# Kernel tuning notes

Hardware: AMD Instinct MI355X
Metric: run time of the kernel (lower is better)

Reference implementation:

```python
import jax, jax.numpy as jnp
import numpy as np

N_NODES = 100000
N_EDGES = 1000000
F_IN = 128
HID = 128
OUT = 64


def setup_inputs() -> dict:
    key = jax.random.key(0)
    ks = jax.random.split(key, 8)
    node_features = jax.random.normal(ks[0], (N_NODES, F_IN), dtype=jnp.float32)
    edge_index = jax.random.randint(ks[1], (2, N_EDGES), 0, N_NODES, dtype=jnp.int64)
    s1 = 1.0 / np.sqrt(F_IN)
    s2 = 1.0 / np.sqrt(HID)
    W1 = jax.random.uniform(ks[2], (F_IN, HID), jnp.float32, -s1, s1)
    b1 = jax.random.uniform(ks[3], (HID,), jnp.float32, -s1, s1)
    W2 = jax.random.uniform(ks[4], (HID, HID), jnp.float32, -s2, s2)
    b2 = jax.random.uniform(ks[5], (HID,), jnp.float32, -s2, s2)
    Wp = jax.random.uniform(ks[6], (HID, OUT), jnp.float32, -s2, s2)
    bp = jax.random.uniform(ks[7], (OUT,), jnp.float32, -s2, s2)
    return {"node_features": node_features, "edge_index": edge_index,
            "W1": W1, "b1": b1, "W2": W2, "b2": b2, "Wp": Wp, "bp": bp}


def reference(node_features, edge_index, W1, b1, W2, b2, Wp, bp):
    # encoder: Linear -> ReLU -> Linear
    h = jax.nn.relu(node_features @ W1 + b1) @ W2 + b2  # [N, HID]
    src = edge_index[0]
    dst = edge_index[1]
    # per-edge gather of h[src], scatter-add into dst (segment reduce)
    messages = jax.ops.segment_sum(h[src], dst, num_segments=h.shape[0])  # [N, HID]
    h = h + messages
    pooled = jnp.mean(h, axis=0)  # [HID]
    return pooled @ Wp + bp  # [OUT]
```

## Files before the change

### kernel.cpp

```cpp
#include <hip/hip_runtime.h>
#include <hip/hip_bf16.h>
#include <stdint.h>

typedef __attribute__((ext_vector_type(8))) short short8;
typedef __attribute__((ext_vector_type(4))) float f32x4;
typedef __attribute__((ext_vector_type(2))) float f32x2;
typedef __attribute__((ext_vector_type(4))) int i32x4;

#define NRANGE 4
#define RNODES 25600
#define RW     12800
#define NS     32
#define NFRAG  16

static __device__ __forceinline__ short to_bf16s(float f) {
  __hip_bfloat16 h = __float2bfloat16(f);
  return __builtin_bit_cast(short, h);
}

__global__ __launch_bounds__(1024) void k_histprep(
    const int* __restrict__ e, unsigned* __restrict__ priv,
    short* __restrict__ frag, const float* __restrict__ W1, int E) {
  __shared__ unsigned cnt[RW];
  __shared__ int is64s;
  int b = blockIdx.x, tid = threadIdx.x;
  if (b < NFRAG) {
    int idx = b * 1024 + tid;
    int k = idx >> 7, col = idx & 127;
    int ct = col >> 4, ks = k >> 5, lh = (k >> 3) & 3, ee = k & 7;
    int lane = lh * 16 + (col & 15);
    frag[((ct * 4 + ks) * 64 + lane) * 8 + ee] = to_bf16s(W1[idx]);
    return;
  }
  int h = b - NFRAG;
  int r = h / NS, s = h % NS;
  if (tid < 64) {
    unsigned long long bl = __ballot(e[2 * tid + 1] == 0);
    if (tid == 0) is64s = (__popcll(bl) > 32) ? 1 : 0;
  }
  for (int j = tid; j < RW; j += 1024) cnt[j] = 0u;
  __syncthreads();
  int is64 = is64s;
  unsigned base = (unsigned)r * RNODES;
  int nq = E >> 2;
  int qlo = (int)((long long)s * nq / NS);
  int qhi = (int)((long long)(s + 1) * nq / NS);
  for (int q = qlo + tid; q < qhi; q += 1024) {
    i32x4 v;
    if (is64) {
      i32x4 a = *reinterpret_cast<const i32x4*>(e + 8 * (size_t)q);
      i32x4 bb = *reinterpret_cast<const i32x4*>(e + 8 * (size_t)q + 4);
      v = i32x4{a[0], a[2], bb[0], bb[2]};
    } else {
      v = *reinterpret_cast<const i32x4*>(e + 4 * (size_t)q);
    }
#pragma unroll
    for (int k = 0; k < 4; ++k) {
      unsigned loc = (unsigned)v[k] - base;
      if (loc < (unsigned)RNODES)
        atomicAdd(&cnt[loc >> 1], 1u << (16 * (loc & 1)));
    }
  }
  if (s == 0) {
    int tail = E & 3;
    if (tid < tail) {
      int idx = E - tail + tid;
      unsigned loc = (unsigned)(is64 ? e[2 * idx] : e[idx]) - base;
      if (loc < (unsigned)RNODES)
        atomicAdd(&cnt[loc >> 1], 1u << (16 * (loc & 1)));
    }
  }
  __syncthreads();
  unsigned* dst = priv + (size_t)h * RW;
  for (int j = tid; j < RW; j += 1024) dst[j] = cnt[j];
}

__global__ __launch_bounds__(256) void k_merge(const unsigned* __restrict__ priv,
                                               float* __restrict__ wdeg, int N) {
  int g = blockIdx.x * 256 + threadIdx.x;
  if (g >= NRANGE * RW) return;
  int r = g / RW, word = g % RW;
  const unsigned* p = priv + (size_t)(r * NS) * RW + word;
  unsigned lo = 0, hi = 0;
#pragma unroll 8
  for (int s = 0; s < NS; ++s) {
    unsigned v = p[(size_t)s * RW];
    lo += v & 0xFFFFu;
    hi += v >> 16;
  }
  int n0 = r * RNODES + 2 * word;
  if (n0 + 1 < N) {
    *reinterpret_cast<f32x2*>(wdeg + n0) =
        f32x2{1.0f + (float)lo, 1.0f + (float)hi};
  } else if (n0 < N) {
    wdeg[n0] = 1.0f + (float)lo;
  }
}

__global__ __launch_bounds__(256) void k_main(
    const float* __restrict__ X, const short* __restrict__ w1frag,
    const float* __restrict__ b1, const float* __restrict__ wdeg,
    float* __restrict__ partials, int nNodes) {
  __shared__ __align__(16) short w1s[16384];
  __shared__ __align__(16) short xs[8192];
  __shared__ float wdeg_s[64];
  __shared__ float sred[128];

  int tid = threadIdx.x;
  {
    const f32x4* src = reinterpret_cast<const f32x4*>(w1frag);
    f32x4* dst = reinterpret_cast<f32x4*>(w1s);
#pragma unroll
    for (int i = 0; i < 8; ++i) dst[tid + i * 256] = src[tid + i * 256];
  }
  if (tid < 128) sred[tid] = 0.f;

  int lane = tid & 63, wave = tid >> 6;
  int rA = lane & 15;
  int kh = lane >> 4;

  float b1r[8];
#pragma unroll
  for (int ct = 0; ct < 8; ++ct) b1r[ct] = b1[ct * 16 + rA];

  float sl[8] = {0, 0, 0, 0, 0, 0, 0, 0};
  int nChunks = (nNodes + 63) >> 6;
  __syncthreads();

  for (int c = blockIdx.x; c < nChunks; c += gridDim.x) {
    int row0 = c << 6;
#pragma unroll
    for (int p = 0; p < 4; ++p) {
      int j = p * 256 + tid;
      int rl = j >> 4, kc = j & 15;
      int grow = row0 + rl;
      if (grow > nNodes - 1) grow = nNodes - 1;
      const f32x4* gp =
          reinterpret_cast<const f32x4*>(X + (size_t)grow * 128 + kc * 8);
      f32x4 lo = gp[0], hi = gp[1];
      short8 v;
#pragma unroll
      for (int ee = 0; ee < 4; ++ee) {
        v[ee] = to_bf16s(lo[ee]);
        v[4 + ee] = to_bf16s(hi[ee]);
      }
      int u = rl * 16 + (kc ^ (rl & 7));
      *reinterpret_cast<short8*>(&xs[u * 8]) = v;
    }
    if (tid < 64) {
      int row = row0 + tid;
      wdeg_s[tid] = (row < nNodes) ? wdeg[row] : 0.f;
    }
    __syncthreads();

    int rloc = wave * 16 + rA;
    f32x4 acc[8];
#pragma unroll
    for (int ct = 0; ct < 8; ++ct) acc[ct] = f32x4{0.f, 0.f, 0.f, 0.f};
#pragma unroll
    for (int ks = 0; ks < 4; ++ks) {
      int kc = ks * 4 + kh;
      int u = rloc * 16 + (kc ^ (rloc & 7));
      short8 a = *reinterpret_cast<const short8*>(&xs[u * 8]);
#pragma unroll
      for (int ct = 0; ct < 8; ++ct) {
        short8 bfr = *reinterpret_cast<const short8*>(
            &w1s[((ct * 4 + ks) * 64 + lane) * 8]);
        acc[ct] = __builtin_amdgcn_mfma_f32_16x16x32_bf16(a, bfr, acc[ct], 0, 0, 0);
      }
    }
#pragma unroll
    for (int rr = 0; rr < 4; ++rr) {
      int rl = wave * 16 + kh * 4 + rr;
      float w = wdeg_s[rl];
#pragma unroll
      for (int ct = 0; ct < 8; ++ct)
        sl[ct] += w * fmaxf(acc[ct][rr] + b1r[ct], 0.f);
    }
    __syncthreads();
  }

#pragma unroll
  for (int ct = 0; ct < 8; ++ct) {
    float v = sl[ct];
    v += __shfl_xor(v, 16);
    v += __shfl_xor(v, 32);
    if (kh == 0) atomicAdd(&sred[ct * 16 + rA], v);
  }
  __syncthreads();
  if (tid < 128) partials[(size_t)blockIdx.x * 128 + tid] = sred[tid];
}

__global__ __launch_bounds__(1024) void k_final(
    const float* __restrict__ partials, int B, const float* __restrict__ W2,
    const float* __restrict__ b2, const float* __restrict__ Wp,
    const float* __restrict__ bp, float* __restrict__ out,
    float totalW, float invN) {
  __shared__ float accsA[32 * 128];
  __shared__ float sv[128];
  __shared__ float pooled[128];
  int t = threadIdx.x;
  {
    int cg = t & 31, slc = t >> 5;
    f32x4 s = f32x4{0.f, 0.f, 0.f, 0.f};
#pragma unroll 4
    for (int r = slc; r < B; r += 32)
      s += *reinterpret_cast<const f32x4*>(partials + (size_t)r * 128 + cg * 4);
    *reinterpret_cast<f32x4*>(&accsA[slc * 128 + cg * 4]) = s;
  }
  __syncthreads();
  if (t < 128) {
    float v = 0.f;
#pragma unroll
    for (int i = 0; i < 32; ++i) v += accsA[i * 128 + t];
    sv[t] = v;
  }
  __syncthreads();
  {
    int col = t & 127, sl8 = t >> 7;
    float a = 0.f;
#pragma unroll
    for (int kk = 0; kk < 16; ++kk) {
      int k = sl8 * 16 + kk;
      a += sv[k] * W2[k * 128 + col];
    }
    accsA[sl8 * 128 + col] = a;
  }
  __syncthreads();
  if (t < 128) {
    float v = totalW * b2[t];
#pragma unroll
    for (int i = 0; i < 8; ++i) v += accsA[i * 128 + t];
    pooled[t] = v * invN;
  }
  __syncthreads();
  if (t < 512) {
    int o = t & 63, s2 = t >> 6;
    float a = 0.f;
#pragma unroll
    for (int kk = 0; kk < 16; ++kk) {
      int k = s2 * 16 + kk;
      a += pooled[k] * Wp[k * 64 + o];
    }
    accsA[s2 * 64 + o] = a;
  }
  __syncthreads();
  if (t < 64) {
    float v = bp[t];
#pragma unroll
    for (int i = 0; i < 8; ++i) v += accsA[i * 64 + t];
    out[t] = v;
  }
}

__global__ void k_zero(unsigned* __restrict__ p, int n) {
  int i = blockIdx.x * 256 + threadIdx.x;
  if (i < n) p[i] = 0u;
}
__global__ __launch_bounds__(256) void k_hist_fb(const int* __restrict__ e,
                                                 unsigned* __restrict__ deg,
                                                 int E) {
  __shared__ int is64s;
  int tid = threadIdx.x;
  if (tid < 64) {
    unsigned long long bl = __ballot(e[2 * tid + 1] == 0);
    if (tid == 0) is64s = (__popcll(bl) > 32) ? 1 : 0;
  }
  __syncthreads();
  int is64 = is64s;
  int stride = gridDim.x * blockDim.x;
  for (int i = blockIdx.x * blockDim.x + tid; i < E; i += stride)
    atomicAdd(&deg[is64 ? (unsigned)e[2 * i] : (unsigned)e[i]], 1u);
}
__global__ void k_cvt(const unsigned* __restrict__ deg,
                      float* __restrict__ wdeg, int N) {
  int i = blockIdx.x * 256 + threadIdx.x;
  if (i < N) wdeg[i] = 1.0f + (float)deg[i];
}

extern "C" void kernel_launch(void* const* d_in, const int* in_sizes, int n_in,
                              void* d_out, int out_size, void* d_ws, size_t ws_size,
                              hipStream_t stream) {
  const float* X  = (const float*)d_in[0];
  const int*   ei = (const int*)d_in[1];
  const float* W1 = (const float*)d_in[2];
  const float* b1 = (const float*)d_in[3];
  const float* W2 = (const float*)d_in[4];
  const float* b2 = (const float*)d_in[5];
  const float* Wp = (const float*)d_in[6];
  const float* bp = (const float*)d_in[7];

  int N = in_sizes[0] / 128;
  int E = in_sizes[1] / 2;
  int nChunks = (N + 63) >> 6;
  int mb = nChunks < 521 ? nChunks : 521;

  size_t privB = (size_t)NRANGE * NS * RW * 4;
  size_t fragB = (16384 * 2 + 255) & ~(size_t)255;
  size_t wdegB = ((size_t)N * 4 + 255) & ~(size_t)255;
  size_t partB = ((size_t)mb * 128 * 4 + 255) & ~(size_t)255;
  size_t fixed = privB + fragB + wdegB + partB + 512;

  bool fast = (N <= NRANGE * RNODES) && (E / NS <= 65000) && (ws_size >= fixed);

  char* p = (char*)d_ws;
  unsigned* priv = (unsigned*)p;  p += privB;
  short* frag = (short*)p;        p += fragB;
  float* wdeg = (float*)p;        p += wdegB;
  float* parts = (float*)p;

  if (fast) {
    k_histprep<<<NFRAG + NRANGE * NS, 1024, 0, stream>>>(ei, priv, frag, W1, E);
    k_merge<<<(NRANGE * RW + 255) / 256, 256, 0, stream>>>(priv, wdeg, N);
  } else {
    k_histprep<<<NFRAG, 1024, 0, stream>>>(ei, priv, frag, W1, E);
    k_zero<<<(N + 255) / 256, 256, 0, stream>>>((unsigned*)wdeg, N);
    k_hist_fb<<<2048, 256, 0, stream>>>(ei, (unsigned*)wdeg, E);
    k_cvt<<<(N + 255) / 256, 256, 0, stream>>>((unsigned*)wdeg, wdeg, N);
  }
  k_main<<<mb, 256, 0, stream>>>(X, frag, b1, wdeg, parts, N);
  k_final<<<1, 1024, 0, stream>>>(parts, mb, W2, b2, Wp, bp, (float*)d_out,
                                  (float)N + (float)E, 1.0f / (float)N);
}
```

Baseline: 37.02 us.

## Fuse degree merge into main kernel and raise grid size with occupancy hint

Removes the separate k_merge launch. k_main now sums the 32 private 16-bit-packed histogram slices for its 64-row chunk directly while it stages X. The grid cap grows from 521 to 782 blocks and launch_bounds requests 3 blocks per CU. This saves one kernel launch and the wdeg round trip through global memory. In exchange, 64 threads per chunk do 32 strided loads each, and the occupancy hint may constrain register allocation.

Result: slower. 40.39 us (+9.1%).

```diff
diff --git a/kernel.cpp b/kernel.cpp
--- a/kernel.cpp
+++ b/kernel.cpp
@@ -4,7 +4,6 @@
 
 typedef __attribute__((ext_vector_type(8))) short short8;
 typedef __attribute__((ext_vector_type(4))) float f32x4;
-typedef __attribute__((ext_vector_type(2))) float f32x2;
 typedef __attribute__((ext_vector_type(4))) int i32x4;
 
 #define NRANGE 4
@@ -75,32 +74,11 @@
   for (int j = tid; j < RW; j += 1024) dst[j] = cnt[j];
 }
 
-__global__ __launch_bounds__(256) void k_merge(const unsigned* __restrict__ priv,
-                                               float* __restrict__ wdeg, int N) {
-  int g = blockIdx.x * 256 + threadIdx.x;
-  if (g >= NRANGE * RW) return;
-  int r = g / RW, word = g % RW;
-  const unsigned* p = priv + (size_t)(r * NS) * RW + word;
-  unsigned lo = 0, hi = 0;
-#pragma unroll 8
-  for (int s = 0; s < NS; ++s) {
-    unsigned v = p[(size_t)s * RW];
-    lo += v & 0xFFFFu;
-    hi += v >> 16;
-  }
-  int n0 = r * RNODES + 2 * word;
-  if (n0 + 1 < N) {
-    *reinterpret_cast<f32x2*>(wdeg + n0) =
-        f32x2{1.0f + (float)lo, 1.0f + (float)hi};
-  } else if (n0 < N) {
-    wdeg[n0] = 1.0f + (float)lo;
-  }
-}
-
-__global__ __launch_bounds__(256) void k_main(
+__global__ __launch_bounds__(256, 3) void k_main(
     const float* __restrict__ X, const short* __restrict__ w1frag,
-    const float* __restrict__ b1, const float* __restrict__ wdeg,
-    float* __restrict__ partials, int nNodes) {
+    const float* __restrict__ b1, const unsigned* __restrict__ privM,
+    const float* __restrict__ wdegG, float* __restrict__ partials,
+    int nNodes) {
   __shared__ __align__(16) short w1s[16384];
   __shared__ __align__(16) short xs[8192];
   __shared__ float wdeg_s[64];
@@ -149,7 +127,19 @@
     }
     if (tid < 64) {
       int row = row0 + tid;
-      wdeg_s[tid] = (row < nNodes) ? wdeg[row] : 0.f;
+      if (privM) {
+        int r = row0 / RNODES;
+        int w = ((row0 - r * RNODES) >> 1) + (tid >> 1);
+        const unsigned* pp = privM + (size_t)(r * NS) * RW + w;
+        unsigned sh = 16u * (tid & 1);
+        unsigned sum = 0;
+#pragma unroll
+        for (int s = 0; s < NS; ++s)
+          sum += (pp[(size_t)s * RW] >> sh) & 0xFFFFu;
+        wdeg_s[tid] = (row < nNodes) ? 1.0f + (float)sum : 0.f;
+      } else {
+        wdeg_s[tid] = (row < nNodes) ? wdegG[row] : 0.f;
+      }
     }
     __syncthreads();
 
@@ -293,7 +283,7 @@
   int N = in_sizes[0] / 128;
   int E = in_sizes[1] / 2;
   int nChunks = (N + 63) >> 6;
-  int mb = nChunks < 521 ? nChunks : 521;
+  int mb = nChunks < 782 ? nChunks : 782;
 
   size_t privB = (size_t)NRANGE * NS * RW * 4;
   size_t fragB = (16384 * 2 + 255) & ~(size_t)255;
@@ -311,14 +301,16 @@
 
   if (fast) {
     k_histprep<<<NFRAG + NRANGE * NS, 1024, 0, stream>>>(ei, priv, frag, W1, E);
-    k_merge<<<(NRANGE * RW + 255) / 256, 256, 0, stream>>>(priv, wdeg, N);
+    k_main<<<mb, 256, 0, stream>>>(X, frag, b1, priv, (const float*)nullptr,
+                                   parts, N);
   } else {
     k_histprep<<<NFRAG, 1024, 0, stream>>>(ei, priv, frag, W1, E);
     k_zero<<<(N + 255) / 256, 256, 0, stream>>>((unsigned*)wdeg, N);
     k_hist_fb<<<2048, 256, 0, stream>>>(ei, (unsigned*)wdeg, E);
     k_cvt<<<(N + 255) / 256, 256, 0, stream>>>((unsigned*)wdeg, wdeg, N);
-  }
-  k_main<<<mb, 256, 0, stream>>>(X, frag, b1, wdeg, parts, N);
+    k_main<<<mb, 256, 0, stream>>>(X, frag, b1, (const unsigned*)nullptr,
+                                   wdeg, parts, N);
+  }
   k_final<<<1, 1024, 0, stream>>>(parts, mb, W2, b2, Wp, bp, (float*)d_out,
                                   (float)N + (float)E, 1.0f / (float)N);
 }
```

## Prefetch next node chunk into registers during MFMA and halve histogram ranges

Applied to the files above, without the earlier changes.

The encoder loop now loads the next 64-row chunk of X and its degree weight into registers before running the MFMA compute on the current chunk, then converts to bf16 and writes it to shared memory afterward. This is meant to hide global load latency behind the matrix work. The histogram configuration also moves to 2 node ranges of 51200 with a larger shared count array, and NS grows to 64. In exchange, register pressure rises, an extra barrier is added per iteration, and the larger LDS footprint may reduce occupancy in the histogram kernel.

New measurement: 37.59 us. No clear change (+1.5%).

```diff
diff --git a/kernel.cpp b/kernel.cpp
--- a/kernel.cpp
+++ b/kernel.cpp
@@ -7,10 +7,10 @@
 typedef __attribute__((ext_vector_type(2))) float f32x2;
 typedef __attribute__((ext_vector_type(4))) int i32x4;
 
-#define NRANGE 4
-#define RNODES 25600
-#define RW     12800
-#define NS     32
+#define NRANGE 2
+#define RNODES 51200
+#define RW     25600
+#define NS     64
 #define NFRAG  16
 
 static __device__ __forceinline__ short to_bf16s(float f) {
@@ -125,33 +125,57 @@
 
   float sl[8] = {0, 0, 0, 0, 0, 0, 0, 0};
   int nChunks = (nNodes + 63) >> 6;
-  __syncthreads();
-
-  for (int c = blockIdx.x; c < nChunks; c += gridDim.x) {
-    int row0 = c << 6;
-#pragma unroll
-    for (int p = 0; p < 4; ++p) {
-      int j = p * 256 + tid;
-      int rl = j >> 4, kc = j & 15;
-      int grow = row0 + rl;
-      if (grow > nNodes - 1) grow = nNodes - 1;
-      const f32x4* gp =
-          reinterpret_cast<const f32x4*>(X + (size_t)grow * 128 + kc * 8);
-      f32x4 lo = gp[0], hi = gp[1];
-      short8 v;
-#pragma unroll
-      for (int ee = 0; ee < 4; ++ee) {
-        v[ee] = to_bf16s(lo[ee]);
-        v[4 + ee] = to_bf16s(hi[ee]);
-      }
-      int u = rl * 16 + (kc ^ (rl & 7));
-      *reinterpret_cast<short8*>(&xs[u * 8]) = v;
-    }
-    if (tid < 64) {
-      int row = row0 + tid;
-      wdeg_s[tid] = (row < nNodes) ? wdeg[row] : 0.f;
-    }
-    __syncthreads();
+  int stride = gridDim.x;
+
+  f32x4 rlo[4], rhi[4];
+  float wreg = 0.f;
+
+#define LOAD_CHUNK(cc)                                                        \
+  {                                                                           \
+    int row0_ = (cc) << 6;                                                    \
+    _Pragma("unroll") for (int p = 0; p < 4; ++p) {                           \
+      int j = p * 256 + tid;                                                  \
+      int rl = j >> 4, kc = j & 15;                                           \
+      int grow = row0_ + rl;                                                  \
+      if (grow > nNodes - 1) grow = nNodes - 1;                               \
+      const f32x4* gp =                                                       \
+          reinterpret_cast<const f32x4*>(X + (size_t)grow * 128 + kc * 8);    \
+      rlo[p] = gp[0];                                                         \
+      rhi[p] = gp[1];                                                         \
+    }                                                                         \
+    if (tid < 64) {                                                           \
+      int row_ = row0_ + tid;                                                 \
+      wreg = (row_ < nNodes) ? wdeg[row_] : 0.f;                              \
+    }                                                                         \
+  }
+
+#define WRITE_CHUNK()                                                         \
+  {                                                                           \
+    _Pragma("unroll") for (int p = 0; p < 4; ++p) {                           \
+      int j = p * 256 + tid;                                                  \
+      int rl = j >> 4, kc = j & 15;                                           \
+      short8 v;                                                               \
+      _Pragma("unroll") for (int ee = 0; ee < 4; ++ee) {                      \
+        v[ee] = to_bf16s(rlo[p][ee]);                                         \
+        v[4 + ee] = to_bf16s(rhi[p][ee]);                                     \
+      }                                                                       \
+      int u = rl * 16 + (kc ^ (rl & 7));                                      \
+      *reinterpret_cast<short8*>(&xs[u * 8]) = v;                             \
+    }                                                                         \
+    if (tid < 64) wdeg_s[tid] = wreg;                                         \
+  }
+
+  int c = blockIdx.x;
+  __syncthreads();
+  if (c < nChunks) {
+    LOAD_CHUNK(c);
+    WRITE_CHUNK();
+  }
+  __syncthreads();
+
+  while (c < nChunks) {
+    int cn = c + stride;
+    if (cn < nChunks) LOAD_CHUNK(cn);
 
     int rloc = wave * 16 + rA;
     f32x4 acc[8];
@@ -178,6 +202,9 @@
         sl[ct] += w * fmaxf(acc[ct][rr] + b1r[ct], 0.f);
     }
     __syncthreads();
+    if (cn < nChunks) WRITE_CHUNK();
+    __syncthreads();
+    c = cn;
   }
 
 #pragma unroll
@@ -189,6 +216,8 @@
   }
   __syncthreads();
   if (tid < 128) partials[(size_t)blockIdx.x * 128 + tid] = sred[tid];
+#undef LOAD_CHUNK
+#undef WRITE_CHUNK
 }
 
 __global__ __launch_bounds__(1024) void k_final(
```
